# Optimization experiments

Measured on AMD Instinct MI355X. Metric: run time of the kernel, lower is better.

## Reference

```python
import jax, jax.numpy as jnp
import numpy as np
from jax import lax

B, L, D_MODEL = 4, 512, 256
N_LAYERS = 6
EXPAND = 2
D_INNER = EXPAND * D_MODEL  # 512
D_STATE = 16
D_CONV = 4
DT_RANK = (D_MODEL + 15) // 16  # 16
EPS = 1e-5


def silu(x):
    return x * jax.nn.sigmoid(x)


def rmsnorm(x, w):
    var = jnp.mean(x * x, axis=-1, keepdims=True)
    return x * lax.rsqrt(var + EPS) * w


def setup_inputs() -> dict:
    key = jax.random.key(0)
    ks = jax.random.split(key, 12)
    s = lambda *sh: 0.02
    inp = {
        "x": jax.random.normal(ks[0], (B, L, D_MODEL), dtype=jnp.float32),
        "norm_w": jnp.ones((N_LAYERS, D_MODEL), jnp.float32),
        "W_in": jax.random.normal(ks[1], (N_LAYERS, 2 * D_INNER, D_MODEL), jnp.float32) * 0.02,
        "b_in": jnp.zeros((N_LAYERS, 2 * D_INNER), jnp.float32),
        "conv_w": jax.random.normal(ks[2], (N_LAYERS, D_INNER, D_CONV), jnp.float32) * 0.2,
        "W_x": jax.random.normal(ks[3], (N_LAYERS, DT_RANK + 2 * D_STATE, D_INNER), jnp.float32) * 0.02,
        "dt_w": jax.random.normal(ks[4], (N_LAYERS, D_INNER, DT_RANK), jnp.float32) * 0.1,
        "dt_b": jax.random.uniform(ks[5], (N_LAYERS, D_INNER), jnp.float32, -4.0, -2.0),
        "A_log": jnp.log(jnp.broadcast_to(jnp.arange(1, D_STATE + 1, dtype=jnp.float32), (N_LAYERS, D_INNER, D_STATE))),
        "D": jnp.ones((N_LAYERS, D_INNER), jnp.float32),
        "W_out": jax.random.normal(ks[6], (N_LAYERS, D_MODEL, D_INNER), jnp.float32) * 0.02,
        "b_out": jnp.zeros((N_LAYERS, D_MODEL), jnp.float32),
    }
    return inp


def mamba_block(x, W_in, b_in, conv_w, W_x, dt_w, dt_b, A_log, D, W_out, b_out):
    # input projection -> (B, L, 2*d_inner)
    xz = jnp.einsum("bld,ed->ble", x, W_in) + b_in
    xin, z = xz[..., :D_INNER], xz[..., D_INNER:]
    # depthwise causal conv over time (groups = d_inner, left pad d_conv-1)
    xc = lax.conv_general_dilated(
        xin.transpose(0, 2, 1),            # (B, C, L)
        conv_w[:, None, :],                # (C, 1, K)
        window_strides=(1,),
        padding=[(D_CONV - 1, 0)],
        feature_group_count=D_INNER,
        dimension_numbers=("NCH", "OIH", "NCH"),
    ).transpose(0, 2, 1)
    u = silu(xc)                           # (B, L, d_inner)
    # data-dependent dt, B, C
    xdbc = jnp.einsum("bld,rd->blr", u, W_x)
    dt = xdbc[..., :DT_RANK]
    Bm = xdbc[..., DT_RANK:DT_RANK + D_STATE]
    Cm = xdbc[..., DT_RANK + D_STATE:]
    delta = jax.nn.softplus(jnp.einsum("blr,dr->bld", dt, dt_w) + dt_b)
    A = -jnp.exp(A_log)                    # (d_inner, d_state)
    dA = jnp.exp(jnp.einsum("bld,dn->bldn", delta, A))
    dBu = jnp.einsum("bld,bln->bldn", delta * u, Bm)
    # selective scan over time
    def step(h, inp):
        dA_t, dBu_t, C_t = inp
        h = dA_t * h + dBu_t               # (B, d_inner, d_state)
        y_t = jnp.einsum("bdn,bn->bd", h, C_t)
        return h, y_t
    h0 = jnp.zeros((B, D_INNER, D_STATE), x.dtype)
    _, ys = lax.scan(step, h0, (dA.transpose(1, 0, 2, 3), dBu.transpose(1, 0, 2, 3), Cm.transpose(1, 0, 2)))
    y = ys.transpose(1, 0, 2) + u * D      # skip connection D*u
    y = y * silu(z)
    return jnp.einsum("bld,md->blm", y, W_out) + b_out


def reference(x, norm_w, W_in, b_in, conv_w, W_x, dt_w, dt_b, A_log, D, W_out, b_out):
    for i in range(N_LAYERS):
        x = x + mamba_block(rmsnorm(x, norm_w[i]), W_in[i], b_in[i], conv_w[i], W_x[i], dt_w[i], dt_b[i], A_log[i], D[i], W_out[i], b_out[i])
    return x
```

## Files before the change

### kernel.cpp

```cpp
#include <hip/hip_runtime.h>
#include <hip/hip_bf16.h>

#define B_SZ 4
#define L_SZ 512
#define D_MODEL 256
#define D_INNER 512
#define D_STATE 16
#define DT_RANK 16
#define N_LAYERS 6
#define BL (B_SZ * L_SZ)

typedef __bf16 bf16_t;
typedef __bf16 bf16x8 __attribute__((ext_vector_type(8)));
typedef __bf16 bf16x4 __attribute__((ext_vector_type(4)));
typedef float  f32x4  __attribute__((ext_vector_type(4)));

__device__ __forceinline__ float row_allreduce16(float x)
{
    int v;
    v = __builtin_amdgcn_mov_dpp(__float_as_int(x), 0x121, 0xf, 0xf, true);
    x += __int_as_float(v);
    v = __builtin_amdgcn_mov_dpp(__float_as_int(x), 0x122, 0xf, 0xf, true);
    x += __int_as_float(v);
    v = __builtin_amdgcn_mov_dpp(__float_as_int(x), 0x124, 0xf, 0xf, true);
    x += __int_as_float(v);
    v = __builtin_amdgcn_mov_dpp(__float_as_int(x), 0x128, 0xf, 0xf, true);
    x += __int_as_float(v);
    return x;
}

__global__ __launch_bounds__(256) void cast3_kernel(
    const float* __restrict__ s0, const float* __restrict__ s1,
    const float* __restrict__ s2, bf16_t* __restrict__ dst,
    int n0, int n1, int n2)
{
    int i = blockIdx.x * 256 + threadIdx.x;
    const float* s; int off;
    if (i < n0)            { s = s0; off = i; }
    else if (i < n0 + n1)  { s = s1; off = i - n0; }
    else if (i < n0+n1+n2) { s = s2; off = i - n0 - n1; }
    else return;
    const float4 v = *(const float4*)(s + (size_t)off * 4);
    bf16x4 o;
    o[0] = (bf16_t)v.x; o[1] = (bf16_t)v.y;
    o[2] = (bf16_t)v.z; o[3] = (bf16_t)v.w;
    *(bf16x4*)(dst + (size_t)i * 4) = o;
}

__global__ __launch_bounds__(256) void rmsnorm_kernel(
    const float* __restrict__ x, const float* __restrict__ w,
    bf16_t* __restrict__ o)
{
    int row  = blockIdx.x * 4 + (threadIdx.x >> 6);
    int lane = threadIdx.x & 63;
    const float4 v = *(const float4*)(x + (size_t)row * D_MODEL + lane * 4);
    float ss = v.x * v.x + v.y * v.y + v.z * v.z + v.w * v.w;
    #pragma unroll
    for (int off = 32; off; off >>= 1) ss += __shfl_xor(ss, off);
    float rs = rsqrtf(ss * (1.f / D_MODEL) + 1e-5f);
    const float4 wv = *(const float4*)(w + lane * 4);
    bf16x4 ov;
    ov[0] = (bf16_t)(v.x * rs * wv.x);
    ov[1] = (bf16_t)(v.y * rs * wv.y);
    ov[2] = (bf16_t)(v.z * rs * wv.z);
    ov[3] = (bf16_t)(v.w * rs * wv.w);
    *(bf16x4*)(o + (size_t)row * D_MODEL + lane * 4) = ov;
}

template<int WM, int WN, int TM_T, int TN_T, int HAS_BIAS, int HAS_RES, int ZSPLIT>
__global__ __launch_bounds__(64 * WM * WN) void gemm_mfma_nt(
    const bf16_t* __restrict__ A, int lda,
    const bf16_t* __restrict__ Bw, int ldb,
    const float* __restrict__ bias,
    const float* __restrict__ R, int ldr,
    float* __restrict__ C, int ldc,
    float* __restrict__ Z,
    int K)
{
    constexpr int BK = 64;
    constexpr int BM = WM * TM_T * 16;
    constexpr int BN = WN * TN_T * 16;
    constexpr int NT = 64 * WM * WN;
    constexpr int LDK = BK + 8;
    __shared__ bf16_t As[BM][LDK];
    __shared__ bf16_t Bs[BN][LDK];

    const int tid  = threadIdx.x;
    const int wave = tid >> 6, lane = tid & 63;
    const int wm = wave / WN, wn = wave % WN;
    const int lm = lane & 15, quad = lane >> 4;
    const int m0 = blockIdx.y * BM, n0 = blockIdx.x * BN;

    f32x4 acc[TM_T][TN_T] = {};

    for (int k0 = 0; k0 < K; k0 += BK) {
        #pragma unroll
        for (int i = tid; i < BM * (BK / 8); i += NT) {
            int r = i >> 3, c8 = i & 7;
            *(bf16x8*)&As[r][c8 * 8] =
                *(const bf16x8*)(A + (size_t)(m0 + r) * lda + k0 + c8 * 8);
        }
        #pragma unroll
        for (int i = tid; i < BN * (BK / 8); i += NT) {
            int r = i >> 3, c8 = i & 7;
            *(bf16x8*)&Bs[r][c8 * 8] =
                *(const bf16x8*)(Bw + (size_t)(n0 + r) * ldb + k0 + c8 * 8);
        }
        __syncthreads();
        #pragma unroll
        for (int ks = 0; ks < BK / 32; ++ks) {
            bf16x8 af[TM_T], bfr[TN_T];
            #pragma unroll
            for (int i = 0; i < TM_T; ++i)
                af[i] = *(const bf16x8*)&As[wm * TM_T * 16 + i * 16 + lm][ks * 32 + quad * 8];
            #pragma unroll
            for (int j = 0; j < TN_T; ++j)
                bfr[j] = *(const bf16x8*)&Bs[wn * TN_T * 16 + j * 16 + lm][ks * 32 + quad * 8];
            #pragma unroll
            for (int i = 0; i < TM_T; ++i)
                #pragma unroll
                for (int j = 0; j < TN_T; ++j)
                    acc[i][j] = __builtin_amdgcn_mfma_f32_16x16x32_bf16(
                        af[i], bfr[j], acc[i][j], 0, 0, 0);
        }
        __syncthreads();
    }

    if (ZSPLIT && n0 >= D_INNER) {
        #pragma unroll
        for (int i = 0; i < TM_T; ++i) {
            int rowbase = m0 + wm * TM_T * 16 + i * 16 + quad * 4;
            #pragma unroll
            for (int j = 0; j < TN_T; ++j) {
                int col = n0 + wn * TN_T * 16 + j * 16 + lm;
                float4 o;
                #pragma unroll
                for (int r = 0; r < 4; ++r) {
                    float v = acc[i][j][r];
                    if (HAS_BIAS) v += bias[col];
                    ((float*)&o)[r] = v / (1.f + __expf(-v));
                }
                *(float4*)(Z + (size_t)(col - D_INNER) * BL + rowbase) = o;
            }
        }
        return;
    }

    #pragma unroll
    for (int i = 0; i < TM_T; ++i) {
        #pragma unroll
        for (int j = 0; j < TN_T; ++j) {
            int col = n0 + wn * TN_T * 16 + j * 16 + lm;
            #pragma unroll
            for (int r = 0; r < 4; ++r) {
                int rowm = m0 + wm * TM_T * 16 + i * 16 + quad * 4 + r;
                float v = acc[i][j][r];
                if (HAS_BIAS) v += bias[col];
                if (HAS_RES)  v += R[(size_t)rowm * ldr + col];
                C[(size_t)rowm * ldc + col] = v;
            }
        }
    }
}

__global__ __launch_bounds__(256) void wx_kernel(
    const bf16_t* __restrict__ A,
    const bf16_t* __restrict__ Bw,
    float* __restrict__ xdbcT)
{
    constexpr int K = 512;
    const int tid  = threadIdx.x;
    const int wave = tid >> 6, lane = tid & 63;
    const int lm = lane & 15, quad = lane >> 4;
    const int m0 = blockIdx.x * 16;

    __shared__ f32x4 part[4][3][64];

    f32x4 acc[3] = {};
    const int kb = wave * 128 + quad * 8;
    #pragma unroll
    for (int ks = 0; ks < 4; ++ks) {
        int k0 = kb + ks * 32;
        bf16x8 af = *(const bf16x8*)(A + (size_t)(m0 + lm) * K + k0);
        #pragma unroll
        for (int j = 0; j < 3; ++j) {
            bf16x8 bfr = *(const bf16x8*)(Bw + (size_t)(j * 16 + lm) * K + k0);
            acc[j] = __builtin_amdgcn_mfma_f32_16x16x32_bf16(af, bfr, acc[j], 0, 0, 0);
        }
    }
    #pragma unroll
    for (int j = 0; j < 3; ++j) part[wave][j][lane] = acc[j];
    __syncthreads();

    if (tid < 192) {
        int j = tid >> 6, l = tid & 63;
        f32x4 s = part[0][j][l];
        s += part[1][j][l];
        s += part[2][j][l];
        s += part[3][j][l];
        int col = j * 16 + (l & 15);
        float4 v = make_float4(s[0], s[1], s[2], s[3]);
        *(float4*)(xdbcT + (size_t)col * BL + m0 + (l >> 4) * 4) = v;
    }
}

__global__ __launch_bounds__(256) void delta_kernel(
    const float* __restrict__ dtT,
    const float* __restrict__ dt_w,
    const float* __restrict__ dt_b,
    float* __restrict__ deltaT)
{
    __shared__ float dts[16][132];

    const int tid = threadIdx.x;
    const int m0  = blockIdx.y * 128;
    const int n   = blockIdx.x * 32 + (tid >> 3);
    const int j   = tid & 7;

    #pragma unroll
    for (int v = 0; v < 2; ++v) {
        int q  = tid + v * 256;
        int k  = q >> 5, mq = q & 31;
        *(float4*)&dts[k][mq * 4] = *(const float4*)(dtT + (size_t)k * BL + m0 + mq * 4);
    }
    __syncthreads();

    float w[16];
    #pragma unroll
    for (int k4 = 0; k4 < 4; ++k4) {
        float4 wv = *(const float4*)(dt_w + (size_t)n * 16 + k4 * 4);
        w[k4*4+0] = wv.x; w[k4*4+1] = wv.y; w[k4*4+2] = wv.z; w[k4*4+3] = wv.w;
    }
    float bv = dt_b[n];

    #pragma unroll
    for (int s = 0; s < 4; ++s) {
        float4 o;
        #pragma unroll
        for (int e = 0; e < 4; ++e) {
            int m = s * 32 + j * 4 + e;
            float a = bv;
            #pragma unroll
            for (int k = 0; k < 16; ++k) a += dts[k][m] * w[k];
            a = (a > 20.f) ? a : __logf(1.f + __expf(a));
            ((float*)&o)[e] = a;
        }
        *(float4*)(deltaT + (size_t)n * BL + m0 + s * 32 + j * 4) = o;
    }
}

__global__ __launch_bounds__(256) void conv_silu_kernel(
    const float* __restrict__ xin, const float* __restrict__ cw,
    float* __restrict__ uT, bf16_t* __restrict__ ub)
{
    int idx = blockIdx.x * 256 + threadIdx.x;
    int d  = idx & (D_INNER - 1);
    int bt = idx >> 9;
    int t  = bt & (L_SZ - 1);
    const float4 wv = *(const float4*)(cw + d * 4);
    const float* base = xin + (size_t)bt * D_INNER + d;
    float acc = wv.w * base[0];
    if (t >= 1) acc += wv.z * base[-D_INNER];
    if (t >= 2) acc += wv.y * base[-2 * D_INNER];
    if (t >= 3) acc += wv.x * base[-3 * D_INNER];
    float s = acc / (1.f + __expf(-acc));
    uT[(size_t)d * BL + bt] = s;
    ub[idx] = (bf16_t)s;
}

__global__ __launch_bounds__(512, 4) void scan_kernel(
    const float* __restrict__ xdbcT,
    const float* __restrict__ deltaT,
    const float* __restrict__ uT,
    const float* __restrict__ szT,
    const float* __restrict__ A_log,
    const float* __restrict__ Dv,
    bf16_t* __restrict__ y)
{
    constexpr int TC = 64;
    constexpr int SC = 16;

    int blk  = blockIdx.x;
    int b    = blk >> 7;
    int dg   = blk & 127;
    int wave = threadIdx.x >> 6;
    int lane = threadIdx.x & 63;
    int d    = dg * 4 + (lane >> 4);
    int n    = lane & 15;

    __shared__ float lds_Ap[8][64];
    __shared__ float lds_he[8][64];

    float Adn = -__expf(A_log[d * D_STATE + n]);
    float Dd  = Dv[d];
    int r0 = b * L_SZ + wave * TC;

    const float* Brow = xdbcT  + (size_t)(DT_RANK + n) * BL;
    const float* Crow = xdbcT  + (size_t)(DT_RANK + D_STATE + n) * BL;
    const float* drow = deltaT + (size_t)d * BL;
    const float* urow = uT     + (size_t)d * BL;
    const float* zrow = szT    + (size_t)d * BL;

    float h = 0.f, Sdl = 0.f;
    for (int t0 = 0; t0 < TC; t0 += SC) {
        float dA[SC], dBu[SC];
        #pragma unroll
        for (int j4 = 0; j4 < SC / 4; ++j4) {
            int rb = r0 + t0 + j4 * 4;
            f32x4 Bv = *(const f32x4*)(Brow + rb);
            f32x4 dl = *(const f32x4*)(drow + rb);
            f32x4 uv = *(const f32x4*)(urow + rb);
            #pragma unroll
            for (int k = 0; k < 4; ++k) {
                dA[j4*4+k]  = __expf(dl[k] * Adn);
                dBu[j4*4+k] = dl[k] * uv[k] * Bv[k];
                Sdl += dl[k];
            }
        }
        #pragma unroll
        for (int j = 0; j < SC; ++j)
            h = dA[j] * h + dBu[j];
    }
    lds_Ap[wave][lane] = __expf(Sdl * Adn);
    lds_he[wave][lane] = h;
    __syncthreads();

    float H = 0.f;
    for (int j = 0; j < wave; ++j)
        H = lds_Ap[j][lane] * H + lds_he[j][lane];

    h = H;
    for (int t0 = 0; t0 < TC; t0 += SC) {
        float dA[SC], dBu[SC], Cv[SC];
        #pragma unroll
        for (int j4 = 0; j4 < SC / 4; ++j4) {
            int rb = r0 + t0 + j4 * 4;
            f32x4 Bv = *(const f32x4*)(Brow + rb);
            f32x4 Cc = *(const f32x4*)(Crow + rb);
            f32x4 dl = *(const f32x4*)(drow + rb);
            f32x4 uv = *(const f32x4*)(urow + rb);
            #pragma unroll
            for (int k = 0; k < 4; ++k) {
                dA[j4*4+k]  = __expf(dl[k] * Adn);
                dBu[j4*4+k] = dl[k] * uv[k] * Bv[k];
                Cv[j4*4+k]  = Cc[k];
            }
        }
        #pragma unroll
        for (int j = 0; j < SC; ++j) {
            h = dA[j] * h + dBu[j];
            Cv[j] = h * Cv[j];
        }
        #pragma unroll
        for (int j = 0; j < SC; ++j)
            Cv[j] = row_allreduce16(Cv[j]);
        if (n == 0) {
            #pragma unroll
            for (int j4 = 0; j4 < SC / 4; ++j4) {
                int rb = r0 + t0 + j4 * 4;
                f32x4 uv = *(const f32x4*)(urow + rb);
                f32x4 sz = *(const f32x4*)(zrow + rb);
                #pragma unroll
                for (int k = 0; k < 4; ++k) {
                    int row = rb + k;
                    y[(size_t)row * D_INNER + d] =
                        (bf16_t)((Cv[j4*4+k] + uv[k] * Dd) * sz[k]);
                }
            }
        }
    }
}

extern "C" void kernel_launch(void* const* d_in, const int* in_sizes, int n_in,
                              void* d_out, int out_size, void* d_ws, size_t ws_size,
                              hipStream_t stream)
{
    const float* x_in   = (const float*)d_in[0];
    const float* norm_w = (const float*)d_in[1];
    const float* W_in   = (const float*)d_in[2];
    const float* b_in   = (const float*)d_in[3];
    const float* conv_w = (const float*)d_in[4];
    const float* W_x    = (const float*)d_in[5];
    const float* dt_w   = (const float*)d_in[6];
    const float* dt_b   = (const float*)d_in[7];
    const float* A_log  = (const float*)d_in[8];
    const float* Dv     = (const float*)d_in[9];
    const float* W_out  = (const float*)d_in[10];
    const float* b_out  = (const float*)d_in[11];
    float* out = (float*)d_out;

    float* ws     = (float*)d_ws;
    float* xz     = ws;
    float* uT     = xz     + BL * D_INNER;
    float* szT    = uT     + D_INNER * BL;
    float* xdbcT  = szT    + D_INNER * BL;
    float* deltaT = xdbcT  + 48 * BL;
    bf16_t* bws   = (bf16_t*)(deltaT + D_INNER * BL);
    bf16_t* xn_bf = bws;
    bf16_t* ub    = xn_bf + BL * D_MODEL;
    bf16_t* y_bf  = ub    + BL * D_INNER;
    bf16_t* Wi_bf = y_bf  + BL * D_INNER;
    bf16_t* Wx_bf = Wi_bf + N_LAYERS * 2 * D_INNER * D_MODEL;
    bf16_t* Wo_bf = Wx_bf + N_LAYERS * 48 * D_INNER;

    {
        int n0 = N_LAYERS * 2 * D_INNER * D_MODEL / 4;
        int n1 = N_LAYERS * 48 * D_INNER / 4;
        int n2 = N_LAYERS * D_MODEL * D_INNER / 4;
        cast3_kernel<<<(n0 + n1 + n2 + 255) / 256, 256, 0, stream>>>(
            W_in, W_x, W_out, Wi_bf, n0, n1, n2);
    }

    for (int i = 0; i < N_LAYERS; ++i) {
        const float* xcur = (i == 0) ? x_in : out;

        rmsnorm_kernel<<<BL / 4, 256, 0, stream>>>(xcur, norm_w + i * D_MODEL, xn_bf);

        gemm_mfma_nt<2, 2, 2, 2, 1, 0, 1><<<dim3(1024 / 64, 2048 / 64), 256, 0, stream>>>(
            xn_bf, D_MODEL, Wi_bf + (size_t)i * 2 * D_INNER * D_MODEL, D_MODEL,
            b_in + i * 2 * D_INNER, nullptr, 0, xz, D_INNER, szT, D_MODEL);

        conv_silu_kernel<<<BL * D_INNER / 256, 256, 0, stream>>>(
            xz, conv_w + i * D_INNER * 4, uT, ub);

        wx_kernel<<<BL / 16, 256, 0, stream>>>(
            ub, Wx_bf + (size_t)i * 48 * D_INNER, xdbcT);

        delta_kernel<<<dim3(16, 16), 256, 0, stream>>>(
            xdbcT, dt_w + (size_t)i * D_INNER * DT_RANK, dt_b + i * D_INNER,
            deltaT);

        scan_kernel<<<512, 512, 0, stream>>>(
            xdbcT, deltaT, uT, szT,
            A_log + (size_t)i * D_INNER * D_STATE, Dv + i * D_INNER, y_bf);

        gemm_mfma_nt<2, 2, 2, 2, 1, 1, 0><<<dim3(256 / 64, 2048 / 64), 256, 0, stream>>>(
            y_bf, D_INNER, Wo_bf + (size_t)i * D_MODEL * D_INNER, D_INNER,
            b_out + i * D_MODEL, xcur, D_MODEL, out, D_MODEL, nullptr, D_INNER);
    }
}
```

Measured before the change: 570.3 us.

## Cache local scan states in registers and shorten chunks with more waves

The scan kernel now keeps each timestep's local state and cumulative decay product in registers during the first pass. The output pass reconstructs h as hl + P*H, so the second sweep no longer reloads B/delta/u, recomputes exp, or runs a serial recurrence. Chunk length is halved to 32 and the block grows to 1024 threads (16 waves), which adds parallelism and shortens the serial chain. In exchange the inter-chunk carry loop is longer, register pressure from the 64 cached floats is higher, and the running product P may lose precision compared with exp of the summed delta.

```diff
diff --git a/kernel.cpp b/kernel.cpp
--- a/kernel.cpp
+++ b/kernel.cpp
@@ -268,7 +268,7 @@
     ub[idx] = (bf16_t)s;
 }
 
-__global__ __launch_bounds__(512, 4) void scan_kernel(
+__global__ __launch_bounds__(1024, 4) void scan_kernel(
     const float* __restrict__ xdbcT,
     const float* __restrict__ deltaT,
     const float* __restrict__ uT,
@@ -277,8 +277,9 @@
     const float* __restrict__ Dv,
     bf16_t* __restrict__ y)
 {
-    constexpr int TC = 64;
-    constexpr int SC = 16;
+    constexpr int TC = 32;
+    constexpr int SC = 8;
+    constexpr int NW = L_SZ / TC;
 
     int blk  = blockIdx.x;
     int b    = blk >> 7;
@@ -288,8 +289,8 @@
     int d    = dg * 4 + (lane >> 4);
     int n    = lane & 15;
 
-    __shared__ float lds_Ap[8][64];
-    __shared__ float lds_he[8][64];
+    __shared__ float lds_Ap[NW][64];
+    __shared__ float lds_he[NW][64];
 
     float Adn = -__expf(A_log[d * D_STATE + n]);
     float Dd  = Dv[d];
@@ -301,7 +302,9 @@
     const float* urow = uT     + (size_t)d * BL;
     const float* zrow = szT    + (size_t)d * BL;
 
-    float h = 0.f, Sdl = 0.f;
+    float hl[TC], Pl[TC];
+    float h = 0.f, P = 1.f;
+    #pragma unroll
     for (int t0 = 0; t0 < TC; t0 += SC) {
         float dA[SC], dBu[SC];
         #pragma unroll
@@ -314,14 +317,17 @@
             for (int k = 0; k < 4; ++k) {
                 dA[j4*4+k]  = __expf(dl[k] * Adn);
                 dBu[j4*4+k] = dl[k] * uv[k] * Bv[k];
-                Sdl += dl[k];
             }
         }
         #pragma unroll
-        for (int j = 0; j < SC; ++j)
+        for (int j = 0; j < SC; ++j) {
             h = dA[j] * h + dBu[j];
-    }
-    lds_Ap[wave][lane] = __expf(Sdl * Adn);
+            P *= dA[j];
+            hl[t0 + j] = h;
+            Pl[t0 + j] = P;
+        }
+    }
+    lds_Ap[wave][lane] = P;
     lds_he[wave][lane] = h;
     __syncthreads();
 
@@ -329,34 +335,25 @@
     for (int j = 0; j < wave; ++j)
         H = lds_Ap[j][lane] * H + lds_he[j][lane];
 
-    h = H;
-    for (int t0 = 0; t0 < TC; t0 += SC) {
-        float dA[SC], dBu[SC], Cv[SC];
-        #pragma unroll
-        for (int j4 = 0; j4 < SC / 4; ++j4) {
+    #pragma unroll
+    for (int t0 = 0; t0 < TC; t0 += 16) {
+        float py[16];
+        #pragma unroll
+        for (int j4 = 0; j4 < 4; ++j4) {
             int rb = r0 + t0 + j4 * 4;
-            f32x4 Bv = *(const f32x4*)(Brow + rb);
             f32x4 Cc = *(const f32x4*)(Crow + rb);
-            f32x4 dl = *(const f32x4*)(drow + rb);
-            f32x4 uv = *(const f32x4*)(urow + rb);
             #pragma unroll
             for (int k = 0; k < 4; ++k) {
-                dA[j4*4+k]  = __expf(dl[k] * Adn);
-                dBu[j4*4+k] = dl[k] * uv[k] * Bv[k];
-                Cv[j4*4+k]  = Cc[k];
+                int t = t0 + j4 * 4 + k;
+                py[j4*4+k] = (hl[t] + Pl[t] * H) * Cc[k];
             }
         }
         #pragma unroll
-        for (int j = 0; j < SC; ++j) {
-            h = dA[j] * h + dBu[j];
-            Cv[j] = h * Cv[j];
-        }
-        #pragma unroll
-        for (int j = 0; j < SC; ++j)
-            Cv[j] = row_allreduce16(Cv[j]);
+        for (int j = 0; j < 16; ++j)
+            py[j] = row_allreduce16(py[j]);
         if (n == 0) {
             #pragma unroll
-            for (int j4 = 0; j4 < SC / 4; ++j4) {
+            for (int j4 = 0; j4 < 4; ++j4) {
                 int rb = r0 + t0 + j4 * 4;
                 f32x4 uv = *(const f32x4*)(urow + rb);
                 f32x4 sz = *(const f32x4*)(zrow + rb);
@@ -364,7 +361,7 @@
                 for (int k = 0; k < 4; ++k) {
                     int row = rb + k;
                     y[(size_t)row * D_INNER + d] =
-                        (bf16_t)((Cv[j4*4+k] + uv[k] * Dd) * sz[k]);
+                        (bf16_t)((py[j4*4+k] + uv[k] * Dd) * sz[k]);
                 }
             }
         }
@@ -430,7 +427,7 @@
             xdbcT, dt_w + (size_t)i * D_INNER * DT_RANK, dt_b + i * D_INNER,
             deltaT);
 
-        scan_kernel<<<512, 512, 0, stream>>>(
+        scan_kernel<<<512, 1024, 0, stream>>>(
             xdbcT, deltaT, uT, szT,
             A_log + (size_t)i * D_INNER * D_STATE, Dv + i * D_INNER, y_bf);
 
```

Result: faster. 523.3 us (-8.3%).
